# Kernel tuning notes

Hardware: AMD Instinct MI355X
Metric: run time of the kernel (lower is better)

Reference implementation:

```python
import jax, jax.numpy as jnp
import numpy as np

B, W, R, D = 2, 4096, 8, 32


def setup_inputs() -> dict:
    key = jax.random.key(0)
    k1, k2, k3 = jax.random.split(key, 3)
    q_alpha = jax.random.normal(k1, (B, W, R), dtype=jnp.float32)
    k = jax.random.normal(k2, (B, W, R), dtype=jnp.float32)
    h_norm = jax.random.normal(k3, (B, W, D), dtype=jnp.float32)
    # RetNet-style decay rates per rank channel: gamma_i = 1 - 2^{-(6+i)} in (0, 1)
    gamma_vec = 1.0 - jnp.exp2(-(6.0 + jnp.arange(R, dtype=jnp.float32)))
    idx = jnp.arange(W)
    decay_diff = (idx[:, None] - idx[None, :]).astype(jnp.float32)  # [W, W], i - j
    causal_mask = (idx[:, None] >= idx[None, :]).astype(jnp.float32)  # [W, W] lower-tri
    return {
        "q_alpha": q_alpha,
        "k": k,
        "h_norm": h_norm,
        "gamma_vec": gamma_vec,
        "causal_mask": causal_mask,
        "decay_diff": decay_diff,
    }


def reference(q_alpha, k, h_norm, gamma_vec, causal_mask, decay_diff):
    # q_alpha, k: [B, W, R]; h_norm: [B, W, D]; gamma_vec: [R]; masks: [W, W]
    window = h_norm.shape[1]
    kh = k[..., :, None] * h_norm[..., None, :]  # [B, W, R, D]
    dist = decay_diff[:window, :window][..., None]  # [W, W, 1]
    log_gamma = jnp.log(jnp.clip(gamma_vec, 1e-8, None)).reshape(1, 1, -1)  # [1, 1, R]
    causal = causal_mask[:window, :window][..., None]  # [W, W, 1]
    decay_mask = jnp.exp(dist * log_gamma) * causal  # [W, W, R]
    causal_inner = jnp.einsum("ijr,bjrd->bird", decay_mask, kh)  # [B, W, R, D]
    return jnp.einsum("bwr,bwrd->bwd", q_alpha, causal_inner)  # [B, W, D]
```

## Files before the change

### kernel.cpp

```cpp
#include <hip/hip_runtime.h>

#define B 2
#define W 4096
#define R 8
#define D 32
#define L 64
#define C (W / L)

__global__ __launch_bounds__(512) void k_local(const float* __restrict__ kin,
                                               const float* __restrict__ hin,
                                               const float* __restrict__ gamma_vec,
                                               float* __restrict__ ws_state) {
    __shared__ float sk[L][R];
    __shared__ float sh[L][D];
    __shared__ float part[2][R][D];
    const int blk = blockIdx.x;
    const int b = blk / C, c = blk % C;
    const int t = threadIdx.x;
    const float* kp = kin + ((size_t)b * W + (size_t)c * L) * R;
    const float* hp = hin + ((size_t)b * W + (size_t)c * L) * D;
    ((float*)sk)[t] = kp[t];
    ((float4*)sh)[t] = ((const float4*)hp)[t];
    __syncthreads();
    const int half = t >> 8;
    const int rd = t & 255;
    const int r = rd >> 5, d = rd & 31;
    const float g = gamma_vec[r];
    const float g2 = g * g;
    float S = 0.f;
#pragma unroll
    for (int m = 0; m < 32; ++m) {
        const int j = 2 * m + half;
        S = S * g2 + sk[j][r] * sh[j][d];
    }
    part[half][r][d] = S;
    __syncthreads();
    if (t < 256) {
        ws_state[(size_t)(b * C + c) * R * D + rd] = part[1][r][d] + g * part[0][r][d];
    }
}

__global__ __launch_bounds__(512) void k_out(const float* __restrict__ qin,
                                             const float* __restrict__ kin,
                                             const float* __restrict__ hin,
                                             const float* __restrict__ gamma_vec,
                                             const float* __restrict__ ws_state,
                                             float* __restrict__ out) {
    __shared__ float sq[L][R + 1];
    __shared__ float sk[L][R];
    __shared__ float sh[L][D];
    __shared__ __align__(16) float sAT[L][L + 4];
    __shared__ float spow[R][L + 1];
    __shared__ float s0[R][D];
    const int blk = blockIdx.x;
    const int b = blk / C, c = blk % C;
    const int t = threadIdx.x;
    const size_t row0 = (size_t)b * W + (size_t)c * L;
    const float* qp = qin + row0 * R;
    const float* kp = kin + row0 * R;
    const float* hp = hin + row0 * D;
    sq[t >> 3][t & 7] = qp[t];
    sk[t >> 3][t & 7] = kp[t];
    ((float4*)sh)[t] = ((const float4*)hp)[t];
    if (t < R) {
        const float g = gamma_vec[t];
        float p = 1.f;
        for (int dl = 0; dl <= L; ++dl) { spow[t][dl] = p; p *= g; }
    }
    __syncthreads();

    if (t < 256) {
        const int r = t >> 5;
        float gL = gamma_vec[r];
#pragma unroll
        for (int s = 0; s < 6; ++s) gL *= gL;
        float P = 0.f;
        const float* wsp = ws_state + (size_t)b * C * R * D + t;
        for (int cc = 0; cc < c; ++cc)
            P = P * gL + wsp[(size_t)cc * R * D];
        s0[r][t & 31] = P;
    }

    for (int e = t; e < L * L; e += 512) {
        const int j = e >> 6, i = e & 63;
        float a = 0.f;
        if (j <= i) {
#pragma unroll
            for (int r = 0; r < R; ++r) a += sq[i][r] * sk[j][r] * spow[r][i - j];
        }
        sAT[j][i] = a;
    }
    __syncthreads();

    const int d = t & 31;
    const int ig = t >> 5;
    float pr[R];
#pragma unroll
    for (int r = 0; r < R; ++r) pr[r] = s0[r][d];
    float acc[4];
#pragma unroll
    for (int s = 0; s < 4; ++s) {
        const int i = ig * 4 + s;
        float a = 0.f;
#pragma unroll
        for (int r = 0; r < R; ++r) a += sq[i][r] * spow[r][i + 1] * pr[r];
        acc[s] = a;
    }
    const int jmax = ig * 4 + 3;
    for (int j = 0; j <= jmax; ++j) {
        const float hv = sh[j][d];
        const float4 av = *(const float4*)&sAT[j][ig * 4];
        acc[0] += av.x * hv; acc[1] += av.y * hv;
        acc[2] += av.z * hv; acc[3] += av.w * hv;
    }
#pragma unroll
    for (int s = 0; s < 4; ++s)
        out[(row0 + (size_t)(ig * 4 + s)) * D + d] = acc[s];
}

extern "C" void kernel_launch(void* const* d_in, const int* in_sizes, int n_in,
                              void* d_out, int out_size, void* d_ws, size_t ws_size,
                              hipStream_t stream) {
    const float* q  = (const float*)d_in[0];
    const float* k  = (const float*)d_in[1];
    const float* h  = (const float*)d_in[2];
    const float* gv = (const float*)d_in[3];
    float* out = (float*)d_out;
    float* ws  = (float*)d_ws;

    k_local<<<B * C, 512, 0, stream>>>(k, h, gv, ws);
    k_out  <<<B * C, 512, 0, stream>>>(q, k, h, gv, ws, out);
}
```

Baseline: 148.0 us.

## Factor decay into per-row q*gamma^i and k*gamma^-j, split warps for state scan

Replaces the per-element gamma^(i-j) table lookup with pre-scaled q (by gamma^i) and k (by gamma^-j) so the intra-chunk score is a plain rank-8 dot product. Threads are split so half load inputs and prescale them while the other half compute the cross-chunk prefix state, with that scan unrolled by 8 to expose memory-level parallelism. The s0 term is folded by one extra gamma so the output path reuses the scaled q directly. It risks precision loss because gamma^-63 grows large for small gamma, though with gamma close to 1 this stays bounded.

```diff
diff --git a/kernel.cpp b/kernel.cpp
--- a/kernel.cpp
+++ b/kernel.cpp
@@ -6,6 +6,17 @@
 #define D 32
 #define L 64
 #define C (W / L)
+
+__device__ __forceinline__ float gpow6(float g, int e) {
+    float p = 1.f;
+    float b = g;
+#pragma unroll
+    for (int bit = 0; bit < 6; ++bit) {
+        p = (e & (1 << bit)) ? p * b : p;
+        b *= b;
+    }
+    return p;
+}
 
 __global__ __launch_bounds__(512) void k_local(const float* __restrict__ kin,
                                                const float* __restrict__ hin,
@@ -46,49 +57,80 @@
                                              const float* __restrict__ gamma_vec,
                                              const float* __restrict__ ws_state,
                                              float* __restrict__ out) {
-    __shared__ float sq[L][R + 1];
-    __shared__ float sk[L][R];
+    __shared__ float sqg[R][L];
+    __shared__ float skg[R][L];
     __shared__ float sh[L][D];
     __shared__ __align__(16) float sAT[L][L + 4];
-    __shared__ float spow[R][L + 1];
     __shared__ float s0[R][D];
     const int blk = blockIdx.x;
     const int b = blk / C, c = blk % C;
     const int t = threadIdx.x;
     const size_t row0 = (size_t)b * W + (size_t)c * L;
-    const float* qp = qin + row0 * R;
-    const float* kp = kin + row0 * R;
-    const float* hp = hin + row0 * D;
-    sq[t >> 3][t & 7] = qp[t];
-    sk[t >> 3][t & 7] = kp[t];
-    ((float4*)sh)[t] = ((const float4*)hp)[t];
-    if (t < R) {
-        const float g = gamma_vec[t];
-        float p = 1.f;
-        for (int dl = 0; dl <= L; ++dl) { spow[t][dl] = p; p *= g; }
+
+    if (t >= 256) {
+        const int u = t - 256;
+        const float* hp = hin + row0 * D;
+        ((float4*)sh)[u]       = ((const float4*)hp)[u];
+        ((float4*)sh)[u + 256] = ((const float4*)hp)[u + 256];
+        const int i = (u & 127) >> 1;
+        const int r0 = (u & 1) * 4;
+        if (u < 128) {
+            const float4 v = ((const float4*)(qin + row0 * R))[u];
+            sqg[r0 + 0][i] = v.x * gpow6(gamma_vec[r0 + 0], i);
+            sqg[r0 + 1][i] = v.y * gpow6(gamma_vec[r0 + 1], i);
+            sqg[r0 + 2][i] = v.z * gpow6(gamma_vec[r0 + 2], i);
+            sqg[r0 + 3][i] = v.w * gpow6(gamma_vec[r0 + 3], i);
+        } else {
+            const float4 v = ((const float4*)(kin + row0 * R))[u - 128];
+            skg[r0 + 0][i] = v.x * gpow6(1.f / gamma_vec[r0 + 0], i);
+            skg[r0 + 1][i] = v.y * gpow6(1.f / gamma_vec[r0 + 1], i);
+            skg[r0 + 2][i] = v.z * gpow6(1.f / gamma_vec[r0 + 2], i);
+            skg[r0 + 3][i] = v.w * gpow6(1.f / gamma_vec[r0 + 3], i);
+        }
+    } else {
+        const int r = t >> 5;
+        const float g = gamma_vec[r];
+        float gL = g;
+#pragma unroll
+        for (int s = 0; s < 6; ++s) gL *= gL;
+        float gp[9];
+        gp[0] = 1.f;
+#pragma unroll
+        for (int e = 1; e <= 8; ++e) gp[e] = gp[e - 1] * gL;
+        float P = 0.f;
+        const float* wsp = ws_state + (size_t)b * C * R * D + t;
+        int cc = 0;
+        const int head = c & 7;
+        for (; cc < head; ++cc) P = P * gL + wsp[(size_t)cc * 256];
+        for (; cc < c; cc += 8) {
+            const float v0 = wsp[(size_t)(cc + 0) * 256];
+            const float v1 = wsp[(size_t)(cc + 1) * 256];
+            const float v2 = wsp[(size_t)(cc + 2) * 256];
+            const float v3 = wsp[(size_t)(cc + 3) * 256];
+            const float v4 = wsp[(size_t)(cc + 4) * 256];
+            const float v5 = wsp[(size_t)(cc + 5) * 256];
+            const float v6 = wsp[(size_t)(cc + 6) * 256];
+            const float v7 = wsp[(size_t)(cc + 7) * 256];
+            const float sg = v0 * gp[7] + v1 * gp[6] + v2 * gp[5] + v3 * gp[4]
+                           + v4 * gp[3] + v5 * gp[2] + v6 * gp[1] + v7;
+            P = P * gp[8] + sg;
+        }
+        s0[r][t & 31] = g * P;
     }
     __syncthreads();
 
-    if (t < 256) {
-        const int r = t >> 5;
-        float gL = gamma_vec[r];
+    const int i = t & 63;
+    const int w = t >> 6;
+    float qreg[R];
 #pragma unroll
-        for (int s = 0; s < 6; ++s) gL *= gL;
-        float P = 0.f;
-        const float* wsp = ws_state + (size_t)b * C * R * D + t;
-        for (int cc = 0; cc < c; ++cc)
-            P = P * gL + wsp[(size_t)cc * R * D];
-        s0[r][t & 31] = P;
-    }
-
-    for (int e = t; e < L * L; e += 512) {
-        const int j = e >> 6, i = e & 63;
+    for (int r = 0; r < R; ++r) qreg[r] = sqg[r][i];
+#pragma unroll
+    for (int p = 0; p < 8; ++p) {
+        const int j = w + 8 * p;
         float a = 0.f;
-        if (j <= i) {
 #pragma unroll
-            for (int r = 0; r < R; ++r) a += sq[i][r] * sk[j][r] * spow[r][i - j];
-        }
-        sAT[j][i] = a;
+        for (int r = 0; r < R; ++r) a += qreg[r] * skg[r][j];
+        sAT[j][i] = (j <= i) ? a : 0.f;
     }
     __syncthreads();
 
@@ -100,10 +142,10 @@
     float acc[4];
 #pragma unroll
     for (int s = 0; s < 4; ++s) {
-        const int i = ig * 4 + s;
+        const int i2 = ig * 4 + s;
         float a = 0.f;
 #pragma unroll
-        for (int r = 0; r < R; ++r) a += sq[i][r] * spow[r][i + 1] * pr[r];
+        for (int r = 0; r < R; ++r) a += sqg[r][i2] * pr[r];
         acc[s] = a;
     }
     const int jmax = ig * 4 + 3;
```

After: 135.7 us. 1.09x faster.
